# Kernel tuning notes

Measured on AMD Instinct MI355X. Metric: run time of the kernel, lower is better.

The kernel has to match this reference:

```python
import jax, jax.numpy as jnp
import numpy as np

B, S, H, NH = 2, 1024, 1024, 16
HD = H // NH          # 64
SP = 0.05             # synaptic_plasticity
EPS = 1e-5            # torch LayerNorm default eps


def setup_inputs() -> dict:
    key = jax.random.key(0)
    ks = jax.random.split(key, 18)
    def lin(k, fin, fout):
        # torch Linear default init ~ U(-1/sqrt(fin), 1/sqrt(fin)); stored as [in, out]
        bound = 1.0 / np.sqrt(fin)
        return jax.random.uniform(k, (fin, fout), jnp.float32, -bound, bound)
    return {
        "query": jax.random.normal(ks[0], (B, S, H), jnp.float32),
        "key_t": jax.random.normal(ks[1], (B, S, H), jnp.float32),
        "value": jax.random.normal(ks[2], (B, S, H), jnp.float32),
        "Wq": lin(ks[3], H, H), "bq": jnp.zeros((H,), jnp.float32),
        "Wk": lin(ks[4], H, H), "bk": jnp.zeros((H,), jnp.float32),
        "Wv": lin(ks[5], H, H), "bv": jnp.zeros((H,), jnp.float32),
        # msb_weights init = ones*0.5 (+ tiny noise so grads are non-degenerate)
        "msb": 0.5 * jnp.ones((NH, HD, HD), jnp.float32)
               + 0.01 * jax.random.normal(ks[6], (NH, HD, HD), jnp.float32),
        "Ws1": lin(ks[7], H, H // 2), "bs1": jnp.zeros((H // 2,), jnp.float32),
        "Ws2": lin(ks[8], H // 2, H), "bs2": jnp.zeros((H,), jnp.float32),
        "Wo": lin(ks[9], H, H), "bo": jnp.zeros((H,), jnp.float32),
        "ln_g": jnp.ones((H,), jnp.float32),
        "ln_b": jnp.zeros((H,), jnp.float32),
    }


def reference(query, key_t, value, Wq, bq, Wk, bk, Wv, bv, msb,
              Ws1, bs1, Ws2, bs2, Wo, bo, ln_g, ln_b):
    b, s, h = query.shape
    # projections -> [b, nh, s, hd]
    Q = (query @ Wq + bq).reshape(b, s, NH, HD).transpose(0, 2, 1, 3)
    K = (key_t @ Wk + bk).reshape(b, s, NH, HD).transpose(0, 2, 1, 3)
    V = (value @ Wv + bv).reshape(b, s, NH, HD).transpose(0, 2, 1, 3)

    scores = jnp.einsum('bhqd,bhkd->bhqk', Q, K) / np.float32(np.sqrt(HD))

    # MSB sigmoid gate: per-head scalar = mean over (head_dim, head_dim)
    msb_h = msb.mean(axis=(1, 2))                              # [NH]
    enh = jax.nn.sigmoid(scores * msb_h[None, :, None, None])  # [b,nh,s,s]
    scores = scores * (1.0 + enh * SP)

    # input-specificity: MLP(mean over seq of query) -> sigmoid -> mean -> scalar per batch
    spec_in = query.mean(axis=1)                               # [b, h]
    h1 = jax.nn.relu(spec_in @ Ws1 + bs1)
    spec = jax.nn.sigmoid(h1 @ Ws2 + bs2).mean(axis=-1)        # [b]
    scores = scores * spec[:, None, None, None]

    w = jax.nn.softmax(scores, axis=-1)                        # dropout p=0 (eval)
    ctx = jnp.einsum('bhqk,bhkd->bhqd', w, V)
    ctx = ctx.transpose(0, 2, 1, 3).reshape(b, s, h)

    out = ctx @ Wo + bo + query                                # residual
    mu = out.mean(axis=-1, keepdims=True)
    var = out.var(axis=-1, keepdims=True)
    return (out - mu) / jnp.sqrt(var + EPS) * ln_g + ln_b
```

## Files before the change

kernel.cpp:

```cpp
#include <hip/hip_runtime.h>
#include <math.h>

#define BB   2
#define SS   1024
#define HH   1024
#define NHH  16
#define SPc  0.05f
#define EPSc 1e-5f

typedef unsigned short u16;
typedef unsigned int   u32;
using bf16x8 = __attribute__((ext_vector_type(8))) __bf16;
using f32x4  = __attribute__((ext_vector_type(4))) float;

__device__ __forceinline__ u16 f2bf(float f) {
    u32 u = __builtin_bit_cast(u32, f);
    u32 r = u + 0x7fffu + ((u >> 16) & 1u);
    return (u16)(r >> 16);
}

__device__ __forceinline__ void async16(void* lds, const void* g) {
    __builtin_amdgcn_global_load_lds((const __attribute__((address_space(1))) u32*)g,
                                     (__attribute__((address_space(3))) u32*)lds,
                                     16, 0, 0);
}

__device__ __forceinline__ bf16x8 ldb8(const u16* p) {
    return *(const bf16x8*)(const void*)p;
}

__global__ __launch_bounds__(256) void prep_kernel(
    const float* __restrict__ query, const float* __restrict__ key_t,
    const float* __restrict__ value,
    u16* __restrict__ Aq, u16* __restrict__ Ak, u16* __restrict__ Av,
    const float* __restrict__ W0, const float* __restrict__ W1,
    const float* __restrict__ W2, const float* __restrict__ W3,
    u16* __restrict__ T0, u16* __restrict__ T1,
    u16* __restrict__ T2, u16* __restrict__ T3,
    const float* __restrict__ msb, float* __restrict__ msbh,
    float* __restrict__ spp) {
    const int t = threadIdx.x;
    const int d = blockIdx.x;

    if (d < 6144) {
        const int which = d >> 11;
        const int bx    = d & 2047;
        const float* s; u16* dst;
        if (which == 0)      { s = query; dst = Aq; }
        else if (which == 1) { s = key_t; dst = Ak; }
        else                 { s = value; dst = Av; }
        const size_t i = ((size_t)bx * 256 + t) * 4;
        const float4 v = *(const float4*)(s + i);
        ushort4 o;
        o.x = f2bf(v.x); o.y = f2bf(v.y); o.z = f2bf(v.z); o.w = f2bf(v.w);
        *(ushort4*)(dst + i) = o;
        return;
    }
    if (d < 7168) {
        const int e  = d - 6144;
        const int wz = e >> 8;
        const int k0 = ((e >> 4) & 15) << 6;
        const int n0 = (e & 15) << 6;
        const float* W; u16* T;
        if (wz == 0)      { W = W0; T = T0; }
        else if (wz == 1) { W = W1; T = T1; }
        else if (wz == 2) { W = W2; T = T2; }
        else              { W = W3; T = T3; }
        __shared__ u16 tile[64][72];
        #pragma unroll
        for (int i = 0; i < 4; ++i) {
            const int chunk = i * 256 + t;
            const int r  = chunk >> 4;
            const int c4 = (chunk & 15) << 2;
            const float4 v = *(const float4*)(W + (size_t)(k0 + r) * 1024 + n0 + c4);
            tile[c4 + 0][r] = f2bf(v.x);
            tile[c4 + 1][r] = f2bf(v.y);
            tile[c4 + 2][r] = f2bf(v.z);
            tile[c4 + 3][r] = f2bf(v.w);
        }
        __syncthreads();
        #pragma unroll
        for (int i = 0; i < 4; ++i) {
            const int chunk = i * 256 + t;
            const int rn = chunk >> 4;
            const int ck = (chunk & 15) << 2;
            ushort4 o;
            o.x = tile[rn][ck + 0];
            o.y = tile[rn][ck + 1];
            o.z = tile[rn][ck + 2];
            o.w = tile[rn][ck + 3];
            *(ushort4*)(T + (size_t)(n0 + rn) * 1024 + k0 + ck) = o;
        }
        return;
    }
    if (d < 7184) {
        const int h = d - 7168;
        const float* p = msb + (size_t)h * 4096;
        float s = 0.f;
        for (int i = t; i < 4096; i += 256) s += p[i];
        __shared__ float red[256];
        red[t] = s;
        __syncthreads();
        for (int off = 128; off > 0; off >>= 1) {
            if (t < off) red[t] += red[t + off];
            __syncthreads();
        }
        if (t == 0) msbh[h] = red[0] * (1.f / 4096.f);
        return;
    }
    {
        const int e = d - 7184;
        const int x = e & 3;
        const int b = (e >> 2) & 1;
        const int z = e >> 3;
        const int h = x * 256 + t;
        const float* p = query + ((size_t)b * SS + (size_t)z * 128) * HH + h;
        float s = 0.f;
        for (int i = 0; i < 128; ++i) s += p[(size_t)i * HH];
        spp[((size_t)z * BB + b) * HH + h] = s;
    }
}

__global__ __launch_bounds__(256) void mlp2_part_kernel(
    const float* __restrict__ mp1, const float* __restrict__ bs1,
    const float* __restrict__ Ws2, float* __restrict__ mp2) {
    const int t   = threadIdx.x;
    const int oc  = blockIdx.x;
    const int kc2 = blockIdx.y;
    const int b   = blockIdx.z;
    __shared__ float x[128];
    if (t < 128) {
        const int j = kc2 * 128 + t;
        float a = bs1[j];
        #pragma unroll
        for (int kc = 0; kc < 8; ++kc) a += mp1[((size_t)kc * BB + b) * 512 + j];
        x[t] = fmaxf(a, 0.f);
    }
    __syncthreads();
    const int o = oc * 256 + t;
    float acc = 0.f;
    #pragma unroll 4
    for (int k2 = 0; k2 < 128; ++k2)
        acc += x[k2] * Ws2[(size_t)(kc2 * 128 + k2) * 1024 + o];
    mp2[((size_t)kc2 * BB + b) * 1024 + o] = acc;
}

template<int BM, int BN>
__device__ __forceinline__ void gemm_core(const u16* __restrict__ A,
                                          const u16* __restrict__ Bt,
                                          const float* __restrict__ bias,
                                          void* __restrict__ Cout, int mode,
                                          int m0, int n0) {
    constexpr int FI = BM / 32;
    constexpr int FJ = BN / 32;
    constexpr int NL = BM / 64 + BN / 64;
    __shared__ u16 sA[3][BM * 32];
    __shared__ u16 sB[3][BN * 32];
    const int t  = threadIdx.x;
    const int l  = t & 63;
    const int wv = t >> 6;
    const int wm = wv >> 1, wn = wv & 1;
    const int wbase = t & ~63;
    const int ql = l & 15;
    const int g_ = l >> 4;

    f32x4 acc[FI][FJ];
    #pragma unroll
    for (int i = 0; i < FI; ++i)
        #pragma unroll
        for (int j = 0; j < FJ; ++j) acc[i][j] = (f32x4){0.f, 0.f, 0.f, 0.f};

    auto stage = [&](int buf, int k0) {
        #pragma unroll
        for (int ii = 0; ii < BM / 64; ++ii) {
            const int chunk = ii * 256 + t;
            const int r  = chunk >> 2, c = chunk & 3;
            const int cs = (c ^ ((r >> 1) & 3)) << 3;
            async16(&sA[buf][(ii * 256 + wbase) << 3],
                    A + (size_t)(m0 + r) * 1024 + k0 + cs);
        }
        #pragma unroll
        for (int ii = 0; ii < BN / 64; ++ii) {
            const int chunk = ii * 256 + t;
            const int r  = chunk >> 2, c = chunk & 3;
            const int cs = (c ^ ((r >> 1) & 3)) << 3;
            async16(&sB[buf][(ii * 256 + wbase) << 3],
                    Bt + (size_t)(n0 + r) * 1024 + k0 + cs);
        }
    };

    stage(0, 0);
    for (int kk = 0; kk < 32; ++kk) {
        const int cur = kk % 3;
        if (kk < 31) {
            stage((kk + 1) % 3, (kk + 1) << 5);
            asm volatile("s_waitcnt vmcnt(%0)" :: "i"(NL) : "memory");
        } else {
            asm volatile("s_waitcnt vmcnt(0)" ::: "memory");
        }
        __builtin_amdgcn_s_barrier();
        const u16* bufA = sA[cur];
        const u16* bufB = sB[cur];
        bf16x8 af[FI], bg[FJ];
        #pragma unroll
        for (int i = 0; i < FI; ++i) {
            const int ra = wm * (BM / 2) + i * 16 + ql;
            af[i] = ldb8(bufA + ra * 32 + (((g_ ^ ((ra >> 1) & 3))) << 3));
        }
        #pragma unroll
        for (int j = 0; j < FJ; ++j) {
            const int rb = wn * (BN / 2) + j * 16 + ql;
            bg[j] = ldb8(bufB + rb * 32 + (((g_ ^ ((rb >> 1) & 3))) << 3));
        }
        __builtin_amdgcn_s_setprio(1);
        #pragma unroll
        for (int i = 0; i < FI; ++i)
            #pragma unroll
            for (int j = 0; j < FJ; ++j)
                acc[i][j] = __builtin_amdgcn_mfma_f32_16x16x32_bf16(af[i], bg[j], acc[i][j], 0, 0, 0);
        __builtin_amdgcn_s_setprio(0);
    }

    const int coll = ql;
    const int rowg = g_ << 2;
    #pragma unroll
    for (int j = 0; j < FJ; ++j) {
        const int n = n0 + wn * (BN / 2) + j * 16 + coll;
        const float bs = bias[n];
        #pragma unroll
        for (int i = 0; i < FI; ++i) {
            const int mb = m0 + wm * (BM / 2) + i * 16 + rowg;
            if (mode == 0) {
                float* C = (float*)Cout;
                #pragma unroll
                for (int rr = 0; rr < 4; ++rr)
                    C[(size_t)(mb + rr) * 1024 + n] = acc[i][j][rr] + bs;
            } else if (mode == 1) {
                u16* C = (u16*)Cout;
                #pragma unroll
                for (int rr = 0; rr < 4; ++rr)
                    C[(size_t)(mb + rr) * 1024 + n] = f2bf(acc[i][j][rr] + bs);
            } else {
                u16* C = (u16*)Cout;
                const int bI = mb >> 10;
                const int s  = mb & 1023;
                ushort4 o;
                o.x = f2bf(acc[i][j][0] + bs);
                o.y = f2bf(acc[i][j][1] + bs);
                o.z = f2bf(acc[i][j][2] + bs);
                o.w = f2bf(acc[i][j][3] + bs);
                *(ushort4*)(C + ((size_t)(bI * NHH + (n >> 6)) * 64 + (n & 63)) * 1024 + s) = o;
            }
        }
    }
}

__global__ __launch_bounds__(256, 3) void gemm_qkv_kernel(
    const u16* __restrict__ Aq, const u16* __restrict__ Ak, const u16* __restrict__ Av,
    const u16* __restrict__ WtQ, const u16* __restrict__ WtK, const u16* __restrict__ WtV,
    const float* __restrict__ bq, const float* __restrict__ bk, const float* __restrict__ bv,
    u16* __restrict__ Qbf, u16* __restrict__ Kbf, u16* __restrict__ Vt,
    const float* __restrict__ spp, const float* __restrict__ Ws1,
    float* __restrict__ mp1) {
    const int d = (int)blockIdx.x;
    if (d >= 768) {
        const int e  = d - 768;
        const int jc = e & 1;
        const int kc = (e >> 1) & 7;
        const int b  = e >> 4;
        const int t  = threadIdx.x;
        __shared__ float x[128];
        if (t < 128) {
            const int k = kc * 128 + t;
            float s = 0.f;
            #pragma unroll
            for (int z = 0; z < 8; ++z) s += spp[((size_t)z * BB + b) * HH + k];
            x[t] = s * (1.f / (float)SS);
        }
        __syncthreads();
        const int j = jc * 256 + t;
        float acc = 0.f;
        #pragma unroll 4
        for (int k2 = 0; k2 < 128; ++k2)
            acc += x[k2] * Ws1[(size_t)(kc * 128 + k2) * 512 + j];
        mp1[((size_t)kc * BB + b) * 512 + j] = acc;
        return;
    }
    const int g = (d & 7) * 96 + (d >> 3);
    const int n0 = (g & 7) << 7;
    const int m0 = ((g >> 3) & 31) << 6;
    const int zz = g >> 8;
    if (zz == 0)      gemm_core<64, 128>(Aq, WtQ, bq, Qbf, 1, m0, n0);
    else if (zz == 1) gemm_core<64, 128>(Ak, WtK, bk, Kbf, 1, m0, n0);
    else              gemm_core<64, 128>(Av, WtV, bv, Vt, 2, m0, n0);
}

__global__ __launch_bounds__(256, 3) void gemm_o_kernel(
    const u16* __restrict__ A, const u16* __restrict__ Bt,
    const float* __restrict__ bias, float* __restrict__ C) {
    const int d = (int)blockIdx.x + ((int)blockIdx.y << 4);
    const int g = (d & 7) * 64 + (d >> 3);
    const int n0 = (g & 15) << 6;
    const int m0 = (g >> 4) << 6;
    gemm_core<64, 64>(A, Bt, bias, C, 0, m0, n0);
}

__global__ __launch_bounds__(256, 2) void attn_mfma_kernel(
    const u16* __restrict__ Qbf, const u16* __restrict__ Kbf,
    const u16* __restrict__ Vt, const float* __restrict__ msbh,
    const float* __restrict__ mp2, const float* __restrict__ bs2,
    u16* __restrict__ ctx) {
    __shared__ u16 sK[3][4096];
    __shared__ u16 sV[3][4096];

    const int t  = threadIdx.x;
    const int l  = t & 63;
    const int wv = t >> 6;
    const int wbase = t & ~63;
    const int qt = blockIdx.x, h = blockIdx.y, b = blockIdx.z;
    const int ql = l & 15;
    const int g_ = l >> 4;

    const u16* Kg = Kbf + (size_t)b * SS * HH + h * 64;
    const u16* Vg = Vt + (size_t)(b * NHH + h) * 64 * SS;

    const u16* qrow = Qbf + ((size_t)(b * SS + qt * 64 + wv * 16 + ql)) * HH + h * 64;
    const bf16x8 qf0 = ldb8(qrow + (g_ << 3));
    const bf16x8 qf1 = ldb8(qrow + ((4 + g_) << 3));

    int koff[2], vof[2], lof[2];
    #pragma unroll
    for (int ii = 0; ii < 2; ++ii) {
        const int chunk = ii * 256 + t;
        const int r = chunk >> 3, c = chunk & 7;
        const int rp = (r & 3) | (((r >> 2) & 3) << 3) | (((r >> 4) & 1) << 2) | (r & 32);
        const int cs = (c ^ (r & 7)) << 3;
        koff[ii] = rp * 1024 + cs;
        vof[ii]  = r * 1024 + cs;
        lof[ii]  = (ii * 256 + wbase) << 3;
    }

#define KVSTAGE(buf, kt)                                                        \
    {                                                                           \
        _Pragma("unroll")                                                       \
        for (int ii = 0; ii < 2; ++ii) {                                        \
            async16(sK[buf] + lof[ii], Kg + ((size_t)(kt) << 16) + koff[ii]);   \
            async16(sV[buf] + lof[ii], Vg + ((kt) << 6) + vof[ii]);             \
        }                                                                       \
    }

    KVSTAGE(0, 0)

    float ssum = 0.f;
    #pragma unroll
    for (int j = 0; j < 16; ++j) {
        const int o = (j << 6) + l;
        float a = bs2[o];
        #pragma unroll
        for (int kc = 0; kc < 4; ++kc) a += mp2[((size_t)kc * BB + b) * 1024 + o];
        ssum += 1.f / (1.f + __expf(-a));
    }
    #pragma unroll
    for (int off = 1; off < 64; off <<= 1) ssum += __shfl_xor(ssum, off);
    const float sp = ssum * (1.f / 1024.f);

    const float mh = msbh[h] * 0.125f;
    const float c2 = 0.125f * sp;
    const float c3 = 0.125f * sp * SPc;
    const float Ac = c2 + 0.5f * c3;
    const float Bc = 0.25f * c3 * mh;
    const float Dc = c3 * mh * mh * mh * (1.f / 48.f);

    f32x4 oacc[4];
    #pragma unroll
    for (int dt = 0; dt < 4; ++dt) oacc[dt] = (f32x4){0.f, 0.f, 0.f, 0.f};
    float lsum = 0.f;

    for (int kt = 0; kt < 16; ++kt) {
        const int cur = kt % 3;
        if (kt < 15) {
            KVSTAGE((kt + 1) % 3, kt + 1)
            asm volatile("s_waitcnt vmcnt(4)" ::: "memory");
        } else {
            asm volatile("s_waitcnt vmcnt(0)" ::: "memory");
        }
        __builtin_amdgcn_s_barrier();

        const u16* bufK = sK[cur];
        const u16* bufV = sV[cur];

        f32x4 sc[4];
        __builtin_amdgcn_s_setprio(1);
        #pragma unroll
        for (int f = 0; f < 4; ++f) {
            const int r = (f << 4) + ql;
            bf16x8 kfa = ldb8(bufK + r * 64 + ((g_ ^ (r & 7)) << 3));
            bf16x8 kfb = ldb8(bufK + r * 64 + (((4 + g_) ^ (r & 7)) << 3));
            f32x4 z = (f32x4){0.f, 0.f, 0.f, 0.f};
            z = __builtin_amdgcn_mfma_f32_16x16x32_bf16(kfa, qf0, z, 0, 0, 0);
            z = __builtin_amdgcn_mfma_f32_16x16x32_bf16(kfb, qf1, z, 0, 0, 0);
            sc[f] = z;
        }
        __builtin_amdgcn_s_setprio(0);

        bf16x8 pf0, pf1;
        #pragma unroll
        for (int f = 0; f < 4; ++f) {
            #pragma unroll
            for (int rr = 0; rr < 4; ++rr) {
                const float raw = sc[f][rr];
                const float r2 = raw * raw;
                const float tt = fmaf(-Dc, r2, Bc);
                const float v  = fmaf(tt, r2, Ac * raw);
                const float p  = __expf(v);
                lsum += p;
                const __bf16 pbv = (__bf16)p;
                if (f == 0)      pf0[rr] = pbv;
                else if (f == 1) pf0[4 + rr] = pbv;
                else if (f == 2) pf1[rr] = pbv;
                else             pf1[4 + rr] = pbv;
            }
        }

        __builtin_amdgcn_s_setprio(1);
        #pragma unroll
        for (int dt = 0; dt < 4; ++dt) {
            const int r = (dt << 4) + ql;
            bf16x8 vf0 = ldb8(bufV + r * 64 + ((g_ ^ (r & 7)) << 3));
            bf16x8 vf1 = ldb8(bufV + r * 64 + (((4 + g_) ^ (r & 7)) << 3));
            oacc[dt] = __builtin_amdgcn_mfma_f32_16x16x32_bf16(pf0, vf0, oacc[dt], 0, 0, 0);
            oacc[dt] = __builtin_amdgcn_mfma_f32_16x16x32_bf16(pf1, vf1, oacc[dt], 0, 0, 0);
        }
        __builtin_amdgcn_s_setprio(0);
    }
#undef KVSTAGE

    lsum += __shfl_xor(lsum, 16);
    lsum += __shfl_xor(lsum, 32);

    float linv[4];
    #pragma unroll
    for (int rr = 0; rr < 4; ++rr) linv[rr] = 1.f / __shfl(lsum, (g_ << 2) + rr);

    #pragma unroll
    for (int rr = 0; rr < 4; ++rr) {
        const int q = qt * 64 + wv * 16 + (g_ << 2) + rr;
        u16* crow = ctx + ((size_t)(b * SS + q)) * HH + h * 64;
        #pragma unroll
        for (int dt = 0; dt < 4; ++dt)
            crow[dt * 16 + ql] = f2bf(oacc[dt][rr] * linv[rr]);
    }
}

__global__ __launch_bounds__(256) void ln_kernel(
    const float* __restrict__ X, const float* __restrict__ qin,
    const float* __restrict__ g, const float* __restrict__ be, float* __restrict__ out) {
    const int row = blockIdx.x;
    const int t   = threadIdx.x;
    const int d4  = t << 2;
    const float4 x4 = *(const float4*)(X + (size_t)row * HH + d4);
    const float4 q4 = *(const float4*)(qin + (size_t)row * HH + d4);
    float4 v;
    v.x = x4.x + q4.x;
    v.y = x4.y + q4.y;
    v.z = x4.z + q4.z;
    v.w = x4.w + q4.w;
    float s  = v.x + v.y + v.z + v.w;
    float sq = v.x * v.x + v.y * v.y + v.z * v.z + v.w * v.w;
    for (int off = 1; off < 64; off <<= 1) {
        s  += __shfl_xor(s, off);
        sq += __shfl_xor(sq, off);
    }
    __shared__ float rs[4], rq[4];
    const int w = t >> 6;
    if ((t & 63) == 0) { rs[w] = s; rq[w] = sq; }
    __syncthreads();
    s  = rs[0] + rs[1] + rs[2] + rs[3];
    sq = rq[0] + rq[1] + rq[2] + rq[3];
    const float mu   = s * (1.f / (float)HH);
    const float var  = sq * (1.f / (float)HH) - mu * mu;
    const float rstd = rsqrtf(var + EPSc);
    const float4 g4 = *(const float4*)(g + d4);
    const float4 b4 = *(const float4*)(be + d4);
    float4 o;
    o.x = (v.x - mu) * rstd * g4.x + b4.x;
    o.y = (v.y - mu) * rstd * g4.y + b4.y;
    o.z = (v.z - mu) * rstd * g4.z + b4.z;
    o.w = (v.w - mu) * rstd * g4.w + b4.w;
    *(float4*)(out + (size_t)row * HH + d4) = o;
}

extern "C" void kernel_launch(void* const* d_in, const int* in_sizes, int n_in,
                              void* d_out, int out_size, void* d_ws, size_t ws_size,
                              hipStream_t stream) {
    (void)in_sizes; (void)n_in; (void)out_size; (void)ws_size;
    const float* query = (const float*)d_in[0];
    const float* key_t = (const float*)d_in[1];
    const float* value = (const float*)d_in[2];
    const float* Wq  = (const float*)d_in[3];
    const float* bq  = (const float*)d_in[4];
    const float* Wk  = (const float*)d_in[5];
    const float* bk  = (const float*)d_in[6];
    const float* Wv  = (const float*)d_in[7];
    const float* bv  = (const float*)d_in[8];
    const float* msb = (const float*)d_in[9];
    const float* Ws1 = (const float*)d_in[10];
    const float* bs1 = (const float*)d_in[11];
    const float* Ws2 = (const float*)d_in[12];
    const float* bs2 = (const float*)d_in[13];
    const float* Wo  = (const float*)d_in[14];
    const float* bo  = (const float*)d_in[15];
    const float* lng = (const float*)d_in[16];
    const float* lnb = (const float*)d_in[17];
    float* out = (float*)d_out;

    char* p = (char*)d_ws;
    u16* Aq    = (u16*)p;
    u16* Ak    = Aq + 2097152;
    u16* Av    = Ak + 2097152;
    u16* WtQ   = Av + 2097152;
    u16* WtK   = WtQ + 1048576;
    u16* WtV   = WtK + 1048576;
    u16* WtO   = WtV + 1048576;
    u16* Qbf   = WtO + 1048576;
    u16* Kbf   = Qbf + 2097152;
    u16* Vt    = Kbf + 2097152;
    u16* ctxbf = Vt + 2097152;
    float* Obuf = (float*)Aq;
    float* spp   = (float*)(p + 36 * 1024 * 1024);
    float* mp1   = spp + 16384;
    float* mp2   = mp1 + 8192;
    float* msbh  = mp2 + 8192;

    prep_kernel<<<dim3(7248), 256, 0, stream>>>(
        query, key_t, value, Aq, Ak, Av,
        Wq, Wk, Wv, Wo, WtQ, WtK, WtV, WtO, msb, msbh, spp);

    gemm_qkv_kernel<<<dim3(800), 256, 0, stream>>>(
        Aq, Ak, Av, WtQ, WtK, WtV, bq, bk, bv, Qbf, Kbf, Vt, spp, Ws1, mp1);

    mlp2_part_kernel<<<dim3(4, 4, BB), 256, 0, stream>>>(mp1, bs1, Ws2, mp2);

    attn_mfma_kernel<<<dim3(16, NHH, BB), 256, 0, stream>>>(
        Qbf, Kbf, Vt, msbh, mp2, bs2, ctxbf);

    gemm_o_kernel<<<dim3(16, 32), 256, 0, stream>>>(ctxbf, WtO, bo, Obuf);

    ln_kernel<<<dim3(BB * SS), 256, 0, stream>>>(Obuf, query, lng, lnb, out);
}
```

Measured before the change: 94.29 us.

## Fuse fp32-to-bf16 input conversion into QKV GEMM LDS loads; use exp2

Drops the separate prep pass that converted query/key/value to bf16. The QKV GEMM now streams fp32 activations straight into LDS with an XOR swizzle and converts them to bf16 when building the MFMA fragments. This removes a full read and write of the three activation tensors, but it doubles the A-side LDS footprint and global load count per stage. The attention softmax also folds log2(e) into its polynomial coefficients and calls exp2f instead of __expf.

```diff
diff --git a/kernel.cpp b/kernel.cpp
--- a/kernel.cpp
+++ b/kernel.cpp
@@ -30,9 +30,7 @@
 }
 
 __global__ __launch_bounds__(256) void prep_kernel(
-    const float* __restrict__ query, const float* __restrict__ key_t,
-    const float* __restrict__ value,
-    u16* __restrict__ Aq, u16* __restrict__ Ak, u16* __restrict__ Av,
+    const float* __restrict__ query,
     const float* __restrict__ W0, const float* __restrict__ W1,
     const float* __restrict__ W2, const float* __restrict__ W3,
     u16* __restrict__ T0, u16* __restrict__ T1,
@@ -42,25 +40,10 @@
     const int t = threadIdx.x;
     const int d = blockIdx.x;
 
-    if (d < 6144) {
-        const int which = d >> 11;
-        const int bx    = d & 2047;
-        const float* s; u16* dst;
-        if (which == 0)      { s = query; dst = Aq; }
-        else if (which == 1) { s = key_t; dst = Ak; }
-        else                 { s = value; dst = Av; }
-        const size_t i = ((size_t)bx * 256 + t) * 4;
-        const float4 v = *(const float4*)(s + i);
-        ushort4 o;
-        o.x = f2bf(v.x); o.y = f2bf(v.y); o.z = f2bf(v.z); o.w = f2bf(v.w);
-        *(ushort4*)(dst + i) = o;
-        return;
-    }
-    if (d < 7168) {
-        const int e  = d - 6144;
-        const int wz = e >> 8;
-        const int k0 = ((e >> 4) & 15) << 6;
-        const int n0 = (e & 15) << 6;
+    if (d < 1024) {
+        const int wz = d >> 8;
+        const int k0 = ((d >> 4) & 15) << 6;
+        const int n0 = (d & 15) << 6;
         const float* W; u16* T;
         if (wz == 0)      { W = W0; T = T0; }
         else if (wz == 1) { W = W1; T = T1; }
@@ -93,8 +76,8 @@
         }
         return;
     }
-    if (d < 7184) {
-        const int h = d - 7168;
+    if (d < 1040) {
+        const int h = d - 1024;
         const float* p = msb + (size_t)h * 4096;
         float s = 0.f;
         for (int i = t; i < 4096; i += 256) s += p[i];
@@ -109,7 +92,7 @@
         return;
     }
     {
-        const int e = d - 7184;
+        const int e = d - 1040;
         const int x = e & 3;
         const int b = (e >> 2) & 1;
         const int z = e >> 3;
@@ -145,16 +128,17 @@
     mp2[((size_t)kc2 * BB + b) * 1024 + o] = acc;
 }
 
-template<int BM, int BN>
-__device__ __forceinline__ void gemm_core(const u16* __restrict__ A,
+template<int BM, int BN, bool AF32>
+__device__ __forceinline__ void gemm_core(const void* __restrict__ Aptr,
                                           const u16* __restrict__ Bt,
                                           const float* __restrict__ bias,
                                           void* __restrict__ Cout, int mode,
                                           int m0, int n0) {
-    constexpr int FI = BM / 32;
-    constexpr int FJ = BN / 32;
-    constexpr int NL = BM / 64 + BN / 64;
-    __shared__ u16 sA[3][BM * 32];
+    constexpr int FI  = BM / 32;
+    constexpr int FJ  = BN / 32;
+    constexpr int AIT = AF32 ? (BM / 32) : (BM / 64);
+    constexpr int NL  = AIT + BN / 64;
+    __shared__ u16 sA[3][AF32 ? BM * 64 : BM * 32];
     __shared__ u16 sB[3][BN * 32];
     const int t  = threadIdx.x;
     const int l  = t & 63;
@@ -172,12 +156,17 @@
 
     auto stage = [&](int buf, int k0) {
         #pragma unroll
-        for (int ii = 0; ii < BM / 64; ++ii) {
+        for (int ii = 0; ii < AIT; ++ii) {
             const int chunk = ii * 256 + t;
-            const int r  = chunk >> 2, c = chunk & 3;
-            const int cs = (c ^ ((r >> 1) & 3)) << 3;
-            async16(&sA[buf][(ii * 256 + wbase) << 3],
-                    A + (size_t)(m0 + r) * 1024 + k0 + cs);
+            if (AF32) {
+                const int r = chunk >> 3, c = chunk & 7;
+                async16(&sA[buf][(ii * 256 + wbase) << 3],
+                        (const float*)Aptr + (size_t)(m0 + r) * 1024 + k0 + ((c ^ (r & 7)) << 2));
+            } else {
+                const int r = chunk >> 2, c = chunk & 3;
+                async16(&sA[buf][(ii * 256 + wbase) << 3],
+                        (const u16*)Aptr + (size_t)(m0 + r) * 1024 + k0 + ((c ^ ((r >> 1) & 3)) << 3));
+            }
         }
         #pragma unroll
         for (int ii = 0; ii < BN / 64; ++ii) {
@@ -199,13 +188,23 @@
             asm volatile("s_waitcnt vmcnt(0)" ::: "memory");
         }
         __builtin_amdgcn_s_barrier();
-        const u16* bufA = sA[cur];
         const u16* bufB = sB[cur];
         bf16x8 af[FI], bg[FJ];
         #pragma unroll
         for (int i = 0; i < FI; ++i) {
             const int ra = wm * (BM / 2) + i * 16 + ql;
-            af[i] = ldb8(bufA + ra * 32 + (((g_ ^ ((ra >> 1) & 3))) << 3));
+            if (AF32) {
+                const float* fA = (const float*)(const void*)&sA[cur][0] + ra * 32;
+                const float4 x0 = *(const float4*)(fA + ((((g_ << 1)    ) ^ (ra & 7)) << 2));
+                const float4 x1 = *(const float4*)(fA + ((((g_ << 1) | 1) ^ (ra & 7)) << 2));
+                bf16x8 v;
+                v[0] = (__bf16)x0.x; v[1] = (__bf16)x0.y; v[2] = (__bf16)x0.z; v[3] = (__bf16)x0.w;
+                v[4] = (__bf16)x1.x; v[5] = (__bf16)x1.y; v[6] = (__bf16)x1.z; v[7] = (__bf16)x1.w;
+                af[i] = v;
+            } else {
+                const u16* bufA = &sA[cur][0];
+                af[i] = ldb8(bufA + ra * 32 + (((g_ ^ ((ra >> 1) & 3))) << 3));
+            }
         }
         #pragma unroll
         for (int j = 0; j < FJ; ++j) {
@@ -256,7 +255,7 @@
 }
 
 __global__ __launch_bounds__(256, 3) void gemm_qkv_kernel(
-    const u16* __restrict__ Aq, const u16* __restrict__ Ak, const u16* __restrict__ Av,
+    const float* __restrict__ Aq, const float* __restrict__ Ak, const float* __restrict__ Av,
     const u16* __restrict__ WtQ, const u16* __restrict__ WtK, const u16* __restrict__ WtV,
     const float* __restrict__ bq, const float* __restrict__ bk, const float* __restrict__ bv,
     u16* __restrict__ Qbf, u16* __restrict__ Kbf, u16* __restrict__ Vt,
@@ -290,9 +289,9 @@
     const int n0 = (g & 7) << 7;
     const int m0 = ((g >> 3) & 31) << 6;
     const int zz = g >> 8;
-    if (zz == 0)      gemm_core<64, 128>(Aq, WtQ, bq, Qbf, 1, m0, n0);
-    else if (zz == 1) gemm_core<64, 128>(Ak, WtK, bk, Kbf, 1, m0, n0);
-    else              gemm_core<64, 128>(Av, WtV, bv, Vt, 2, m0, n0);
+    if (zz == 0)      gemm_core<64, 128, true>(Aq, WtQ, bq, Qbf, 1, m0, n0);
+    else if (zz == 1) gemm_core<64, 128, true>(Ak, WtK, bk, Kbf, 1, m0, n0);
+    else              gemm_core<64, 128, true>(Av, WtV, bv, Vt, 2, m0, n0);
 }
 
 __global__ __launch_bounds__(256, 3) void gemm_o_kernel(
@@ -302,7 +301,7 @@
     const int g = (d & 7) * 64 + (d >> 3);
     const int n0 = (g & 15) << 6;
     const int m0 = (g >> 4) << 6;
-    gemm_core<64, 64>(A, Bt, bias, C, 0, m0, n0);
+    gemm_core<64, 64, false>(A, Bt, bias, C, 0, m0, n0);
 }
 
 __global__ __launch_bounds__(256, 2) void attn_mfma_kernel(
@@ -367,9 +366,10 @@
     const float mh = msbh[h] * 0.125f;
     const float c2 = 0.125f * sp;
     const float c3 = 0.125f * sp * SPc;
-    const float Ac = c2 + 0.5f * c3;
-    const float Bc = 0.25f * c3 * mh;
-    const float Dc = c3 * mh * mh * mh * (1.f / 48.f);
+    constexpr float L2E = 1.44269504088896f;
+    const float Ac = (c2 + 0.5f * c3) * L2E;
+    const float Bc = 0.25f * c3 * mh * L2E;
+    const float Dc = c3 * mh * mh * mh * (1.f / 48.f) * L2E;
 
     f32x4 oacc[4];
     #pragma unroll
@@ -412,7 +412,7 @@
                 const float r2 = raw * raw;
                 const float tt = fmaf(-Dc, r2, Bc);
                 const float v  = fmaf(tt, r2, Ac * raw);
-                const float p  = __expf(v);
+                const float p  = exp2f(v);
                 lsum += p;
                 const __bf16 pbv = (__bf16)p;
                 if (f == 0)      pf0[rr] = pbv;
@@ -515,10 +515,8 @@
     float* out = (float*)d_out;
 
     char* p = (char*)d_ws;
-    u16* Aq    = (u16*)p;
-    u16* Ak    = Aq + 2097152;
-    u16* Av    = Ak + 2097152;
-    u16* WtQ   = Av + 2097152;
+    float* Obuf = (float*)p;
+    u16* WtQ   = (u16*)(p + 12 * 1024 * 1024);
     u16* WtK   = WtQ + 1048576;
     u16* WtV   = WtK + 1048576;
     u16* WtO   = WtV + 1048576;
@@ -526,18 +524,16 @@
     u16* Kbf   = Qbf + 2097152;
     u16* Vt    = Kbf + 2097152;
     u16* ctxbf = Vt + 2097152;
-    float* Obuf = (float*)Aq;
     float* spp   = (float*)(p + 36 * 1024 * 1024);
     float* mp1   = spp + 16384;
     float* mp2   = mp1 + 8192;
     float* msbh  = mp2 + 8192;
 
-    prep_kernel<<<dim3(7248), 256, 0, stream>>>(
-        query, key_t, value, Aq, Ak, Av,
-        Wq, Wk, Wv, Wo, WtQ, WtK, WtV, WtO, msb, msbh, spp);
+    prep_kernel<<<dim3(1104), 256, 0, stream>>>(
+        query, Wq, Wk, Wv, Wo, WtQ, WtK, WtV, WtO, msb, msbh, spp);
 
     gemm_qkv_kernel<<<dim3(800), 256, 0, stream>>>(
-        Aq, Ak, Av, WtQ, WtK, WtV, bq, bk, bv, Qbf, Kbf, Vt, spp, Ws1, mp1);
+        query, key_t, value, WtQ, WtK, WtV, bq, bk, bv, Qbf, Kbf, Vt, spp, Ws1, mp1);
 
     mlp2_part_kernel<<<dim3(4, 4, BB), 256, 0, stream>>>(mp1, bs1, Ws2, mp2);
 
```

New measurement: 102.0 us. +8.2%, slower.
